# Performance work log

Measured on AMD Instinct MI355X. Metric: run time of the kernel, lower is better.

The kernel has to match this reference:

```python
import jax, jax.numpy as jnp
import numpy as np

B, SEQ, K, H = 4096, 50, 4, 64   # batch, seq_len, interest_num, hidden_size
ROUTING_TIMES = 3


def setup_inputs() -> dict:
    key = jax.random.key(0)
    k1, k2, k3 = jax.random.split(key, 3)
    mask = jax.random.randint(k1, (B, SEQ), 0, 2, dtype=jnp.int32)
    item_eb_hat = jax.random.normal(k2, (B, SEQ, K, H), dtype=jnp.float32)
    capsule_weight = jax.random.normal(k3, (B, K, SEQ), dtype=jnp.float32)
    return {"mask": mask, "item_eb_hat": item_eb_hat, "capsule_weight": capsule_weight}


def _squash(v):
    # v: [B, K, 1, H]
    cap_norm = jnp.sum(jnp.square(v), -1, keepdims=True)
    scalar = cap_norm / (1.0 + cap_norm) / jnp.sqrt(cap_norm + 1e-9)
    return scalar * v


def reference(mask, item_eb_hat, capsule_weight):
    # [B, seq, K, H] -> [B, K, seq, H]
    x = jnp.transpose(item_eb_hat.reshape(-1, SEQ, K, H), (0, 2, 1, 3))
    x_iter = jax.lax.stop_gradient(x)  # stop_grad=True in the module
    # attention mask broadcast to [B, K, seq]
    am = jnp.broadcast_to(mask[:, None, :], capsule_weight.shape)
    interest_capsule = None
    for i in range(ROUTING_TIMES):
        # torch F.softmax without dim on a 3D tensor -> dim=0 (batch axis); faithful.
        w = jax.nn.softmax(capsule_weight, axis=0)
        w = jnp.where(am == 0, jnp.zeros_like(w), w)[:, :, None, :]  # [B,K,1,seq]
        if i < ROUTING_TIMES - 1:
            interest_capsule = _squash(jnp.matmul(w, x_iter))          # [B,K,1,H]
            delta = jnp.matmul(x_iter, jnp.swapaxes(interest_capsule, -1, -2))  # [B,K,seq,1]
            capsule_weight = capsule_weight + delta.reshape(-1, K, SEQ)
        else:
            interest_capsule = _squash(jnp.matmul(w, x))               # [B,K,1,H]
    return interest_capsule.reshape(-1, K, H)
```

## Files before the change

kernel.cpp:

```cpp
#include <hip/hip_runtime.h>
#include <math.h>

#define BB 4096
#define SEQ 50
#define KK 4
#define HH 64
#define NCOL (KK*SEQ)
#define NPART 64
#define BPP (BB/NPART)

__device__ __forceinline__ float readlane_f32(float v, int lane) {
    return __int_as_float(__builtin_amdgcn_readlane(__float_as_int(v), lane));
}

__global__ void init_kernel(const float* __restrict__ cw,
                            float* __restrict__ part0,
                            float* __restrict__ part1,
                            float* __restrict__ part2) {
    const int p = blockIdx.x;
    const int t = threadIdx.x;
    if (t < NCOL) {
        const float* row = cw + (size_t)p * BPP * NCOL + t;
        float s = 0.f;
#pragma unroll 8
        for (int b = 0; b < BPP; b++) s += __expf(row[b * NCOL]);
        part0[p * NCOL + t] = s;
        part1[p * NCOL + t] = 0.f;
        part2[p * NCOL + t] = 0.f;
    }
}

template <int ITER>
__global__ void update_kernel(const float* __restrict__ cw_src,
                              float* __restrict__ cw_dst,
                              const float* __restrict__ x,
                              const int* __restrict__ mask,
                              const float* __restrict__ part_in,
                              float* __restrict__ part_out,
                              float* __restrict__ out) {
    const int b = blockIdx.x;
    const int k = threadIdx.x >> 6;
    const int h = threadIdx.x & 63;
    const int hs = (h < SEQ) ? h : 0;

    __shared__ float scol[NCOL];

    if (threadIdx.x < NCOL) {
        float s = 0.f;
#pragma unroll 16
        for (int p = 0; p < NPART; p++) s += part_in[p * NCOL + threadIdx.x];
        scol[threadIdx.x] = s;
    }

    const float c = cw_src[(size_t)b * NCOL + k * SEQ + hs];
    const int  mk = mask[b * SEQ + hs];

    __syncthreads();

    const float e = __expf(c) / scol[k * SEQ + hs];
    const float wlane = (h < SEQ && mk != 0) ? e : 0.f;

    const float* xp = x + (size_t)b * (SEQ * KK * HH) + k * HH + h;
    float v = 0.f;
#pragma unroll
    for (int s = 0; s < SEQ; s++)
        v = fmaf(readlane_f32(wlane, s), xp[s * (KK * HH)], v);

    float n2 = v * v;
#pragma unroll
    for (int off = 32; off >= 1; off >>= 1) n2 += __shfl_xor(n2, off, 64);
    const float scalar = n2 / ((1.f + n2) * sqrtf(n2 + 1e-9f));
    v *= scalar;

    if (ITER == 2) {
        out[(size_t)b * (KK * HH) + k * HH + h] = v;
    } else {
        const float* xt = x + (size_t)b * (SEQ * KK * HH) + hs * (KK * HH) + k * HH;
        float g[16];
#pragma unroll
        for (int j4 = 0; j4 < 16; j4++) {
            const float4 xv = *(const float4*)(xt + j4 * 4);
            const float p0 = xv.x * readlane_f32(v, 4 * j4 + 0);
            const float p1 = xv.y * readlane_f32(v, 4 * j4 + 1);
            const float p2 = xv.z * readlane_f32(v, 4 * j4 + 2);
            const float p3 = xv.w * readlane_f32(v, 4 * j4 + 3);
            g[j4] = (p0 + p1) + (p2 + p3);
        }
        float t8[8], t4[4], t2[2];
#pragma unroll
        for (int i = 0; i < 8; i++) t8[i] = g[2 * i] + g[2 * i + 1];
#pragma unroll
        for (int i = 0; i < 4; i++) t4[i] = t8[2 * i] + t8[2 * i + 1];
#pragma unroll
        for (int i = 0; i < 2; i++) t2[i] = t4[2 * i] + t4[2 * i + 1];
        const float del = t2[0] + t2[1];

        if (h < SEQ) {
            const float nc = c + del;
            cw_dst[(size_t)b * NCOL + k * SEQ + h] = nc;
            atomicAdd(&part_out[(b >> 6) * NCOL + k * SEQ + h], __expf(nc));
        }
    }
}

extern "C" void kernel_launch(void* const* d_in, const int* in_sizes, int n_in,
                              void* d_out, int out_size, void* d_ws, size_t ws_size,
                              hipStream_t stream) {
    const int*   mask  = (const int*)d_in[0];
    const float* x     = (const float*)d_in[1];
    const float* cw_in = (const float*)d_in[2];
    float* out = (float*)d_out;

    float* cw_ws = (float*)d_ws;
    float* part0 = cw_ws + (size_t)BB * NCOL;
    float* part1 = part0 + NPART * NCOL;
    float* part2 = part1 + NPART * NCOL;

    init_kernel<<<NPART, 256, 0, stream>>>(cw_in, part0, part1, part2);
    update_kernel<0><<<BB, 256, 0, stream>>>(cw_in, cw_ws, x, mask, part0, part1, nullptr);
    update_kernel<1><<<BB, 256, 0, stream>>>(cw_ws, cw_ws, x, mask, part1, part2, nullptr);
    update_kernel<2><<<BB, 256, 0, stream>>>(cw_ws, nullptr, x, mask, part2, nullptr, out);
}
```

Measured before the change: 389.4 us.

## Stage x tile in LDS for routing updates and cut softmax partials

The update kernels now copy each batch's 50x256 slice of x into padded LDS once, then read it from LDS for both the weighted sum and the delta dot product, instead of doing two strided global passes. The squashed capsule is exchanged through LDS rather than readlane. The number of partial softmax-denominator buckets drops from 64 to 16, so each thread sums fewer partials directly without a shared reduction, at the cost of more atomic contention per bucket. The final iteration is split into its own kernel that skips the LDS staging. The large LDS footprint (about 52KB per block) may limit occupancy.

```diff
diff --git a/kernel.cpp b/kernel.cpp
--- a/kernel.cpp
+++ b/kernel.cpp
@@ -6,8 +6,9 @@
 #define KK 4
 #define HH 64
 #define NCOL (KK*SEQ)
-#define NPART 64
+#define NPART 16
 #define BPP (BB/NPART)
+#define LDSTRIDE 260
 
 __device__ __forceinline__ float readlane_f32(float v, int lane) {
     return __int_as_float(__builtin_amdgcn_readlane(__float_as_int(v), lane));
@@ -36,28 +37,91 @@
                               const float* __restrict__ x,
                               const int* __restrict__ mask,
                               const float* __restrict__ part_in,
-                              float* __restrict__ part_out,
-                              float* __restrict__ out) {
+                              float* __restrict__ part_out) {
     const int b = blockIdx.x;
     const int k = threadIdx.x >> 6;
     const int h = threadIdx.x & 63;
     const int hs = (h < SEQ) ? h : 0;
 
-    __shared__ float scol[NCOL];
+    __shared__ float lds_x[SEQ * LDSTRIDE];
+    __shared__ float vbuf[KK][HH];
 
-    if (threadIdx.x < NCOL) {
-        float s = 0.f;
-#pragma unroll 16
-        for (int p = 0; p < NPART; p++) s += part_in[p * NCOL + threadIdx.x];
-        scol[threadIdx.x] = s;
+    const float* xg = x + (size_t)b * (SEQ * KK * HH);
+#pragma unroll
+    for (int i = 0; i < 13; i++) {
+        const int idx = i * 256 + threadIdx.x;
+        if (idx < SEQ * 64) {
+            const int r = idx >> 6, c = idx & 63;
+            const float4 g = *(const float4*)(xg + r * (KK * HH) + c * 4);
+            *(float4*)&lds_x[r * LDSTRIDE + c * 4] = g;
+        }
     }
 
-    const float c = cw_src[(size_t)b * NCOL + k * SEQ + hs];
+    const int col = k * SEQ + hs;
+    float den = 0.f;
+#pragma unroll
+    for (int p = 0; p < NPART; p++) den += part_in[p * NCOL + col];
+
+    const float c0 = cw_src[(size_t)b * NCOL + col];
     const int  mk = mask[b * SEQ + hs];
 
     __syncthreads();
 
-    const float e = __expf(c) / scol[k * SEQ + hs];
+    const float e = __expf(c0) / den;
+    const float wlane = (h < SEQ && mk != 0) ? e : 0.f;
+
+    float v = 0.f;
+#pragma unroll
+    for (int s = 0; s < SEQ; s++)
+        v = fmaf(readlane_f32(wlane, s), lds_x[s * LDSTRIDE + k * HH + h], v);
+
+    float n2 = v * v;
+#pragma unroll
+    for (int off = 32; off >= 1; off >>= 1) n2 += __shfl_xor(n2, off, 64);
+    const float scalar = n2 / ((1.f + n2) * sqrtf(n2 + 1e-9f));
+    v *= scalar;
+
+    vbuf[k][h] = v;
+    const float* xrow = &lds_x[hs * LDSTRIDE + k * HH];
+    float g16[16];
+#pragma unroll
+    for (int j4 = 0; j4 < 16; j4++) {
+        const float4 xv = *(const float4*)(xrow + 4 * j4);
+        const float4 vv = *(const float4*)&vbuf[k][4 * j4];
+        g16[j4] = (xv.x * vv.x + xv.y * vv.y) + (xv.z * vv.z + xv.w * vv.w);
+    }
+    float t8[8], t4[4];
+#pragma unroll
+    for (int i = 0; i < 8; i++) t8[i] = g16[2 * i] + g16[2 * i + 1];
+#pragma unroll
+    for (int i = 0; i < 4; i++) t4[i] = t8[2 * i] + t8[2 * i + 1];
+    const float del = (t4[0] + t4[1]) + (t4[2] + t4[3]);
+
+    if (h < SEQ) {
+        const float nc = c0 + del;
+        cw_dst[(size_t)b * NCOL + col] = nc;
+        atomicAdd(&part_out[(b >> 8) * NCOL + col], __expf(nc));
+    }
+}
+
+__global__ void final_kernel(const float* __restrict__ cw_src,
+                             const float* __restrict__ x,
+                             const int* __restrict__ mask,
+                             const float* __restrict__ part_in,
+                             float* __restrict__ out) {
+    const int b = blockIdx.x;
+    const int k = threadIdx.x >> 6;
+    const int h = threadIdx.x & 63;
+    const int hs = (h < SEQ) ? h : 0;
+
+    const int col = k * SEQ + hs;
+    float den = 0.f;
+#pragma unroll
+    for (int p = 0; p < NPART; p++) den += part_in[p * NCOL + col];
+
+    const float c0 = cw_src[(size_t)b * NCOL + col];
+    const int  mk = mask[b * SEQ + hs];
+    const float e = __expf(c0) / den;
     const float wlane = (h < SEQ && mk != 0) ? e : 0.f;
 
     const float* xp = x + (size_t)b * (SEQ * KK * HH) + k * HH + h;
@@ -70,37 +134,7 @@
 #pragma unroll
     for (int off = 32; off >= 1; off >>= 1) n2 += __shfl_xor(n2, off, 64);
     const float scalar = n2 / ((1.f + n2) * sqrtf(n2 + 1e-9f));
-    v *= scalar;
-
-    if (ITER == 2) {
-        out[(size_t)b * (KK * HH) + k * HH + h] = v;
-    } else {
-        const float* xt = x + (size_t)b * (SEQ * KK * HH) + hs * (KK * HH) + k * HH;
-        float g[16];
-#pragma unroll
-        for (int j4 = 0; j4 < 16; j4++) {
-            const float4 xv = *(const float4*)(xt + j4 * 4);
-            const float p0 = xv.x * readlane_f32(v, 4 * j4 + 0);
-            const float p1 = xv.y * readlane_f32(v, 4 * j4 + 1);
-            const float p2 = xv.z * readlane_f32(v, 4 * j4 + 2);
-            const float p3 = xv.w * readlane_f32(v, 4 * j4 + 3);
-            g[j4] = (p0 + p1) + (p2 + p3);
-        }
-        float t8[8], t4[4], t2[2];
-#pragma unroll
-        for (int i = 0; i < 8; i++) t8[i] = g[2 * i] + g[2 * i + 1];
-#pragma unroll
-        for (int i = 0; i < 4; i++) t4[i] = t8[2 * i] + t8[2 * i + 1];
-#pragma unroll
-        for (int i = 0; i < 2; i++) t2[i] = t4[2 * i] + t4[2 * i + 1];
-        const float del = t2[0] + t2[1];
-
-        if (h < SEQ) {
-            const float nc = c + del;
-            cw_dst[(size_t)b * NCOL + k * SEQ + h] = nc;
-            atomicAdd(&part_out[(b >> 6) * NCOL + k * SEQ + h], __expf(nc));
-        }
-    }
+    out[(size_t)b * (KK * HH) + k * HH + h] = v * scalar;
 }
 
 extern "C" void kernel_launch(void* const* d_in, const int* in_sizes, int n_in,
@@ -117,7 +151,7 @@
     float* part2 = part1 + NPART * NCOL;
 
     init_kernel<<<NPART, 256, 0, stream>>>(cw_in, part0, part1, part2);
-    update_kernel<0><<<BB, 256, 0, stream>>>(cw_in, cw_ws, x, mask, part0, part1, nullptr);
-    update_kernel<1><<<BB, 256, 0, stream>>>(cw_ws, cw_ws, x, mask, part1, part2, nullptr);
-    update_kernel<2><<<BB, 256, 0, stream>>>(cw_ws, nullptr, x, mask, part2, nullptr, out);
+    update_kernel<0><<<BB, 256, 0, stream>>>(cw_in, cw_ws, x, mask, part0, part1);
+    update_kernel<1><<<BB, 256, 0, stream>>>(cw_ws, cw_ws, x, mask, part1, part2);
+    final_kernel<<<BB, 256, 0, stream>>>(cw_ws, x, mask, part2, out);
 }
```

New measurement: 424.5 us. +9.0%, slower.
